# Performance work log

Measured on AMD Instinct MI355X. Metric: run time of the kernel, lower is better.

The kernel has to match this reference:

```python
import jax, jax.numpy as jnp
import numpy as np

BLANK = 59  # CFG['pad_phrase'] == blank_index == label pad value
NEG = jnp.float32(-1e30)  # -inf surrogate safe for logaddexp


def setup_inputs() -> dict:
    key = jax.random.key(0)
    k1, k2 = jax.random.split(key)
    B, T, V, L = 1024, 384, 60, 45
    labels = jax.random.randint(k1, (B, L), 0, BLANK, dtype=jnp.int32)
    logits = jax.random.normal(k2, (B, T, V), dtype=jnp.float32)
    return {"labels": labels, "logits": logits}


def _ctc_loss(logits, labels):
    # logits: [B, T, V] (not time-major), labels: [B, L] padded with BLANK
    B, T, V = logits.shape
    L = labels.shape[1]
    S = 2 * L + 1  # extended label length: blanks interleaved

    logp = jax.nn.log_softmax(logits, axis=-1)  # tf.nn.ctc_loss softmaxes internally

    # extended label sequence: [blank, l1, blank, l2, ..., blank]
    ext = jnp.full((B, S), BLANK, dtype=jnp.int32).at[:, 1::2].set(labels)
    # per-step emission log-probs for each extended-label position: [B, T, S]
    emit = jnp.take_along_axis(logp, ext[:, None, :], axis=2)

    # skip transition s-2 -> s allowed iff s >= 2, ext[s] != blank, ext[s] != ext[s-2]
    ext_m2 = jnp.pad(ext[:, :-2], ((0, 0), (2, 0)), constant_values=-1)
    skip_ok = (jnp.arange(S) >= 2) & (ext != BLANK) & (ext != ext_m2)

    # alpha init at t=0: only positions 0 (blank) and 1 (first label) reachable
    alpha0 = jnp.full((B, S), NEG).at[:, 0].set(emit[:, 0, 0]).at[:, 1].set(emit[:, 0, 1])

    def step(alpha, emit_t):
        s1 = jnp.pad(alpha[:, :-1], ((0, 0), (1, 0)), constant_values=NEG)
        s2 = jnp.where(skip_ok, jnp.pad(alpha[:, :-2], ((0, 0), (2, 0)), constant_values=NEG), NEG)
        alpha = jnp.logaddexp(jnp.logaddexp(alpha, s1), s2) + emit_t
        return alpha, None

    emit_tbs = jnp.swapaxes(emit, 0, 1)  # [T, B, S]
    alpha_T, _ = jax.lax.scan(step, alpha0, emit_tbs[1:])

    # label_length = number of non-pad tokens (as in the TF layer)
    label_len = jnp.sum((labels != BLANK).astype(jnp.int32), axis=-1)
    end = 2 * label_len  # index of final blank in extended sequence
    a_blank = jnp.take_along_axis(alpha_T, end[:, None], axis=1)[:, 0]
    a_label = jnp.take_along_axis(alpha_T, jnp.maximum(end - 1, 0)[:, None], axis=1)[:, 0]
    a_label = jnp.where(end > 0, a_label, NEG)
    nll = -jnp.logaddexp(a_blank, a_label)  # [B]
    return jnp.mean(nll)


def reference(labels, logits):
    return _ctc_loss(logits, labels)
```

## Files before the change

### kernel.cpp

```cpp
#include <hip/hip_runtime.h>
#include <hip/hip_fp16.h>

#define BLANKC 59

typedef _Float16 half8 __attribute__((ext_vector_type(8)));

__device__ __forceinline__ float wave_shr1(float x, float fill) {
    int r = __builtin_amdgcn_update_dpp(__float_as_int(fill), __float_as_int(x),
                                        0x138 , 0xF, 0xF, false);
    return __int_as_float(r);
}

template <int CTRL>
__device__ __forceinline__ float dpp_fmax(float x) {
    int r = __builtin_amdgcn_update_dpp(__float_as_int(x), __float_as_int(x),
                                        CTRL, 0xF, 0xF, false);
    return fmaxf(x, __int_as_float(r));
}

__device__ __forceinline__ float wave_max_bcast(float x) {
    x = dpp_fmax<0x111>(x);
    x = dpp_fmax<0x112>(x);
    x = dpp_fmax<0x114>(x);
    x = dpp_fmax<0x118>(x);
    x = dpp_fmax<0x142>(x);
    x = dpp_fmax<0x143>(x);
    return __int_as_float(__builtin_amdgcn_readlane(__float_as_int(x), 63));
}

#define TTILE 64
#define RS 392

__global__ __launch_bounds__(256)
void ctc_fused(const int* __restrict__ labels, const float* __restrict__ logits,
               float* __restrict__ out, int T, int V, int L, float inv_b) {
    const int b   = blockIdx.x;
    const int tid = threadIdx.x;

    __shared__ float  ftile[TTILE][61];
    __shared__ __half S[47 * RS];
    __shared__ int    labs[64];

    if (tid < 64) labs[tid] = (tid < L) ? labels[(long)b * L + tid] : BLANKC;
    for (int i = tid; i < T; i += 256) S[46 * RS + i] = __float2half(0.f);

    const float* src = logits + (long)b * T * V;
    const int ntile = T / TTILE;
    for (int tile = 0; tile < ntile; ++tile) {
        const float* s0 = src + (long)tile * TTILE * V;
        #pragma unroll
        for (int it = 0; it < 15; ++it) {
            const int idx = it * 256 + tid;
            const int r = idx / 60, c = idx - r * 60;
            ftile[r][c] = s0[idx];
        }
        __syncthreads();
        {
            const int t = tid >> 2;
            const int q = tid & 3;
            float s = 0.f;
            #pragma unroll
            for (int k = 0; k < 15; ++k) s += __expf(ftile[t][q * 15 + k]);
            s += __shfl_xor(s, 1, 64);
            s += __shfl_xor(s, 2, 64);
            const float lse = __logf(s);
            const int tg = tile * TTILE + t;
            #pragma unroll
            for (int j = 0; j < 12; ++j) {
                const int l = q * 12 + j;
                if (l < 46) {
                    const int v = (l < 45) ? labs[l] : BLANKC;
                    S[l * RS + tg] = __float2half(__expf(ftile[t][v] - lse));
                }
            }
        }
        __syncthreads();
    }

    if (tid >= 64) return;
    const int lane = tid;

    const int labL = (lane < L) ? labs[lane] : BLANKC;
    const int labP = (lane >= 1 && lane < L) ? labs[lane - 1] : BLANKC;
    const float skipf = ((lane >= 1) && (lane < L) && (labL != BLANKC) && (labL != labP))
                        ? 1.0f : 0.0f;

    unsigned long long mk = __ballot((lane < L) && (labL != BLANKC));
    const int len = __popcll(mk);

    const __half* zrow = &S[46 * RS];
    const __half* rowL = (lane < 45) ? &S[lane * RS] : zrow;
    const __half* rowB = (lane < 46) ? &S[45 * RS] : zrow;

    half8 curL = *(const half8*)(rowL);
    half8 curB = *(const half8*)(rowB);

    float a0 = (lane == 0) ? (float)curB[0] * 0x1p80f : 0.f;
    float a1 = (lane == 0) ? (float)curL[0] * 0x1p80f : 0.f;
    int esum = 80;

    auto step = [&](float eL, float eB) {
        const float p   = wave_shr1(a1, 0.0f);
        const float t1  = a0 + a1;
        const float na0 = (a0 + p) * eB;
        const float na1 = fmaf(skipf, p, t1) * eL;
        a0 = na0; a1 = na1;
    };

    auto renorm = [&]() {
        const float m = wave_max_bcast(fmaxf(a0, a1));
        const int e = (__float_as_int(m) >> 23) & 0xff;
        int sexp = 207 - e;
        if (sexp > 127) sexp = 127;
        const float sc = __int_as_float((sexp + 127) << 23);
        a0 *= sc; a1 *= sc;
        esum += sexp;
    };

    const int NSEG = T / 8;

    half8 nL = *(const half8*)(rowL + 8);
    half8 nB = *(const half8*)(rowB + 8);
    #pragma unroll
    for (int i = 1; i < 8; ++i) step((float)curL[i], (float)curB[i]);
    renorm();

    for (int c = 1; c < NSEG - 1; ++c) {
        const half8 cL = nL, cB = nB;
        nL = *(const half8*)(rowL + (c + 1) * 8);
        nB = *(const half8*)(rowB + (c + 1) * 8);
        #pragma unroll
        for (int i = 0; i < 8; ++i) step((float)cL[i], (float)cB[i]);
        renorm();
    }
    #pragma unroll
    for (int i = 0; i < 8; ++i) step((float)nL[i], (float)nB[i]);

    const float ab2 = __shfl(a0, len, 64);
    float al2 = __shfl(a1, (len > 0) ? len - 1 : 0, 64);
    al2 = (len > 0) ? al2 : 0.f;
    if (lane == 0) {
        const float s   = ab2 + al2;
        const float nll = -(__logf(s) - (float)esum * 0.69314718056f);
        atomicAdd(out, nll * inv_b);
    }
}

extern "C" void kernel_launch(void* const* d_in, const int* in_sizes, int n_in,
                              void* d_out, int out_size, void* d_ws, size_t ws_size,
                              hipStream_t stream) {
    const int* labels   = (const int*)d_in[0];
    const float* logits = (const float*)d_in[1];
    float* out          = (float*)d_out;
    (void)d_ws; (void)ws_size;

    const int L = 45, V = 60;
    const int B = in_sizes[0] / L;
    const int T = in_sizes[1] / (B * V);

    hipMemsetAsync(out, 0, (size_t)out_size * sizeof(float), stream);
    ctc_fused<<<B, 256, 0, stream>>>(labels, logits, out, T, V, L, 1.0f / (float)B);
}
```

Measured before the change: 170.9 us.

## Overlap alpha recursion scan with softmax/gather of next time tile

Restructures the kernel so wave 0 runs the CTC alpha recursion on the current 64-step tile while the whole block loads the next tile's logits into registers and computes log-softmax and the label gather into a double-buffered shared tile. Before, all emissions for the full sequence were computed first and the single-wave scan ran afterwards, leaving the other waves idle. The shared emission buffer also shrinks from the full T length to two 64-step tiles, which may raise occupancy. The cost is extra barriers per tile, and the scan in wave 0 now shares its critical path with the load and gather work in that same wave.

```diff
diff --git a/kernel.cpp b/kernel.cpp
--- a/kernel.cpp
+++ b/kernel.cpp
@@ -29,75 +29,66 @@
 }
 
 #define TTILE 64
-#define RS 392
+#define SDS 72
 
 __global__ __launch_bounds__(256)
 void ctc_fused(const int* __restrict__ labels, const float* __restrict__ logits,
                float* __restrict__ out, int T, int V, int L, float inv_b) {
-    const int b   = blockIdx.x;
-    const int tid = threadIdx.x;
+    const int b    = blockIdx.x;
+    const int tid  = threadIdx.x;
+    const int lane = tid & 63;
+    const int wid  = tid >> 6;
 
     __shared__ float  ftile[TTILE][61];
-    __shared__ __half S[47 * RS];
+    __shared__ __half Sd[2][47][SDS];
     __shared__ int    labs[64];
 
     if (tid < 64) labs[tid] = (tid < L) ? labels[(long)b * L + tid] : BLANKC;
-    for (int i = tid; i < T; i += 256) S[46 * RS + i] = __float2half(0.f);
+    if (tid < SDS) {
+        Sd[0][46][tid] = __float2half(0.f);
+        Sd[1][46][tid] = __float2half(0.f);
+    }
 
     const float* src = logits + (long)b * T * V;
     const int ntile = T / TTILE;
-    for (int tile = 0; tile < ntile; ++tile) {
-        const float* s0 = src + (long)tile * TTILE * V;
+
+    float rg[15];
+    auto load_tile = [&](int kt) {
+        const float* s0 = src + (long)kt * TTILE * V;
+        #pragma unroll
+        for (int it = 0; it < 15; ++it) rg[it] = s0[it * 256 + tid];
+    };
+    auto ftile_write = [&]() {
         #pragma unroll
         for (int it = 0; it < 15; ++it) {
             const int idx = it * 256 + tid;
             const int r = idx / 60, c = idx - r * 60;
-            ftile[r][c] = s0[idx];
+            ftile[r][c] = rg[it];
         }
-        __syncthreads();
-        {
-            const int t = tid >> 2;
-            const int q = tid & 3;
-            float s = 0.f;
-            #pragma unroll
-            for (int k = 0; k < 15; ++k) s += __expf(ftile[t][q * 15 + k]);
-            s += __shfl_xor(s, 1, 64);
-            s += __shfl_xor(s, 2, 64);
-            const float lse = __logf(s);
-            const int tg = tile * TTILE + t;
-            #pragma unroll
-            for (int j = 0; j < 12; ++j) {
-                const int l = q * 12 + j;
-                if (l < 46) {
-                    const int v = (l < 45) ? labs[l] : BLANKC;
-                    S[l * RS + tg] = __float2half(__expf(ftile[t][v] - lse));
-                }
+    };
+    auto lse_gather = [&](int nb) {
+        const int t = tid >> 2;
+        const int q = tid & 3;
+        float s = 0.f;
+        #pragma unroll
+        for (int k = 0; k < 15; ++k) s += __expf(ftile[t][q * 15 + k]);
+        s += __shfl_xor(s, 1, 64);
+        s += __shfl_xor(s, 2, 64);
+        const float lse = __logf(s);
+        #pragma unroll
+        for (int j = 0; j < 12; ++j) {
+            const int l = q * 12 + j;
+            if (l < 46) {
+                const int v = (l < 45) ? labs[l] : BLANKC;
+                Sd[nb][l][t] = __float2half(__expf(ftile[t][v] - lse));
             }
         }
-        __syncthreads();
-    }
+    };
 
-    if (tid >= 64) return;
-    const int lane = tid;
-
-    const int labL = (lane < L) ? labs[lane] : BLANKC;
-    const int labP = (lane >= 1 && lane < L) ? labs[lane - 1] : BLANKC;
-    const float skipf = ((lane >= 1) && (lane < L) && (labL != BLANKC) && (labL != labP))
-                        ? 1.0f : 0.0f;
-
-    unsigned long long mk = __ballot((lane < L) && (labL != BLANKC));
-    const int len = __popcll(mk);
-
-    const __half* zrow = &S[46 * RS];
-    const __half* rowL = (lane < 45) ? &S[lane * RS] : zrow;
-    const __half* rowB = (lane < 46) ? &S[45 * RS] : zrow;
-
-    half8 curL = *(const half8*)(rowL);
-    half8 curB = *(const half8*)(rowB);
-
-    float a0 = (lane == 0) ? (float)curB[0] * 0x1p80f : 0.f;
-    float a1 = (lane == 0) ? (float)curL[0] * 0x1p80f : 0.f;
-    int esum = 80;
+    float a0 = 0.f, a1 = 0.f;
+    int esum = 0;
+    float skipf = 0.f;
+    int len = 0, riL = 46, riB = 46;
 
     auto step = [&](float eL, float eB) {
         const float p   = wave_shr1(a1, 0.0f);
@@ -106,7 +97,6 @@
         const float na1 = fmaf(skipf, p, t1) * eL;
         a0 = na0; a1 = na1;
     };
-
     auto renorm = [&]() {
         const float m = wave_max_bcast(fmaxf(a0, a1));
         const int e = (__float_as_int(m) >> 23) & 0xff;
@@ -116,25 +106,67 @@
         a0 *= sc; a1 *= sc;
         esum += sexp;
     };
+    auto scan_tile = [&](int cb, bool first) {
+        const __half* rl = &Sd[cb][riL][0];
+        const __half* rb = &Sd[cb][riB][0];
+        half8 cL = *(const half8*)rl;
+        half8 cB = *(const half8*)rb;
+        half8 nL = *(const half8*)(rl + 8);
+        half8 nB = *(const half8*)(rb + 8);
+        if (first) {
+            a0 = (lane == 0) ? (float)cB[0] * 0x1p80f : 0.f;
+            a1 = (lane == 0) ? (float)cL[0] * 0x1p80f : 0.f;
+            esum = 80;
+            #pragma unroll
+            for (int i = 1; i < 8; ++i) step((float)cL[i], (float)cB[i]);
+        } else {
+            #pragma unroll
+            for (int i = 0; i < 8; ++i) step((float)cL[i], (float)cB[i]);
+        }
+        renorm();
+        #pragma unroll
+        for (int c = 1; c < 8; ++c) {
+            cL = nL; cB = nB;
+            if (c < 7) {
+                nL = *(const half8*)(rl + (c + 1) * 8);
+                nB = *(const half8*)(rb + (c + 1) * 8);
+            }
+            #pragma unroll
+            for (int i = 0; i < 8; ++i) step((float)cL[i], (float)cB[i]);
+            renorm();
+        }
+    };
 
-    const int NSEG = T / 8;
+    load_tile(0);
+    __syncthreads();
+    ftile_write();
+    __syncthreads();
+    lse_gather(0);
 
-    half8 nL = *(const half8*)(rowL + 8);
-    half8 nB = *(const half8*)(rowB + 8);
-    #pragma unroll
-    for (int i = 1; i < 8; ++i) step((float)curL[i], (float)curB[i]);
-    renorm();
+    {
+        const int labL = (lane < L) ? labs[lane] : BLANKC;
+        const int labP = (lane >= 1 && lane < L) ? labs[lane - 1] : BLANKC;
+        skipf = ((lane >= 1) && (lane < L) && (labL != BLANKC) && (labL != labP))
+                ? 1.0f : 0.0f;
+        const unsigned long long mk = __ballot((lane < L) && (labL != BLANKC));
+        len = __popcll(mk);
+        riL = (lane < 45) ? lane : 46;
+        riB = (lane < 46) ? 45 : 46;
+    }
+    __syncthreads();
 
-    for (int c = 1; c < NSEG - 1; ++c) {
-        const half8 cL = nL, cB = nB;
-        nL = *(const half8*)(rowL + (c + 1) * 8);
-        nB = *(const half8*)(rowB + (c + 1) * 8);
-        #pragma unroll
-        for (int i = 0; i < 8; ++i) step((float)cL[i], (float)cB[i]);
-        renorm();
+    int cur = 0;
+    for (int kt = 0; kt < ntile - 1; ++kt) {
+        load_tile(kt + 1);
+        if (wid == 0) scan_tile(cur, kt == 0);
+        ftile_write();
+        __syncthreads();
+        lse_gather(cur ^ 1);
+        __syncthreads();
+        cur ^= 1;
     }
-    #pragma unroll
-    for (int i = 0; i < 8; ++i) step((float)nL[i], (float)nB[i]);
+    if (wid != 0) return;
+    scan_tile(cur, ntile == 1);
 
     const float ab2 = __shfl(a0, len, 64);
     float al2 = __shfl(a1, (len > 0) ? len - 1 : 0, 64);
```

Result: faster. 153.3 us (-10.3%).

## Overlap softmax producer waves with CTC recursion via LDS flags

Applied to the files above, without the earlier changes.

Splits the block into three producer waves that compute softmax on 8-timestep chunks and one consumer wave that runs the alpha recursion as soon as each chunk is flagged ready, instead of finishing all softmax work before the serial recursion starts. The softmax uses a reciprocal and direct exp ratio instead of log/exp, vectorised float4 loads with register prefetch, and an XOR-swizzled emission layout to reduce bank conflicts. It adds spin-waiting on LDS atomics with memory fences, and hardcodes T=384 (NCH=48, 3 waves of 128 steps) and V=60.

```diff
diff --git a/kernel.cpp b/kernel.cpp
--- a/kernel.cpp
+++ b/kernel.cpp
@@ -4,6 +4,7 @@
 #define BLANKC 59
 
 typedef _Float16 half8 __attribute__((ext_vector_type(8)));
+typedef _Float16 half4 __attribute__((ext_vector_type(4)));
 
 __device__ __forceinline__ float wave_shr1(float x, float fill) {
     int r = __builtin_amdgcn_update_dpp(__float_as_int(fill), __float_as_int(x),
@@ -16,6 +17,13 @@
     int r = __builtin_amdgcn_update_dpp(__float_as_int(x), __float_as_int(x),
                                         CTRL, 0xF, 0xF, false);
     return fmaxf(x, __int_as_float(r));
+}
+
+template <int CTRL>
+__device__ __forceinline__ float dpp_addf(float x) {
+    int r = __builtin_amdgcn_update_dpp(__float_as_int(x), __float_as_int(x),
+                                        CTRL, 0xF, 0xF, false);
+    return x + __int_as_float(r);
 }
 
 __device__ __forceinline__ float wave_max_bcast(float x) {
@@ -28,76 +36,108 @@
     return __int_as_float(__builtin_amdgcn_readlane(__float_as_int(x), 63));
 }
 
-#define TTILE 64
-#define RS 392
+#define RS   392
+#define NCH  48
+#define SCRS 68
 
 __global__ __launch_bounds__(256)
 void ctc_fused(const int* __restrict__ labels, const float* __restrict__ logits,
                float* __restrict__ out, int T, int V, int L, float inv_b) {
-    const int b   = blockIdx.x;
-    const int tid = threadIdx.x;
-
-    __shared__ float  ftile[TTILE][61];
-    __shared__ __half S[47 * RS];
-    __shared__ int    labs[64];
+    const int b    = blockIdx.x;
+    const int tid  = threadIdx.x;
+    const int lane = tid & 63;
+    const int wid  = tid >> 6;
+
+    __shared__ __align__(16) __half S[46 * RS];
+    __shared__ __align__(16) __half scr[3][8][SCRS];
+    __shared__ int labs[64];
+    __shared__ int flags[4];
 
     if (tid < 64) labs[tid] = (tid < L) ? labels[(long)b * L + tid] : BLANKC;
-    for (int i = tid; i < T; i += 256) S[46 * RS + i] = __float2half(0.f);
-
-    const float* src = logits + (long)b * T * V;
-    const int ntile = T / TTILE;
-    for (int tile = 0; tile < ntile; ++tile) {
-        const float* s0 = src + (long)tile * TTILE * V;
+    if (tid < 4)  flags[tid] = 0;
+    __syncthreads();
+
+    if (wid != 0) {
+        const int w  = wid - 1;
+        const int tq = lane >> 3;
+        const int q  = lane & 7;
+        const int c0 = q * 8;
+        const bool full = (q < 7);
+        const float* src = logits + (long)b * T * V;
+
+        int gl[6], gr[6], gv[6]; bool gok[6];
         #pragma unroll
-        for (int it = 0; it < 15; ++it) {
-            const int idx = it * 256 + tid;
-            const int r = idx / 60, c = idx - r * 60;
-            ftile[r][c] = s0[idx];
-        }
-        __syncthreads();
-        {
-            const int t = tid >> 2;
-            const int q = tid & 3;
-            float s = 0.f;
+        for (int k = 0; k < 6; ++k) {
+            const int i = lane + (k << 6);
+            gok[k] = (i < 368);
+            gl[k] = i >> 3; gr[k] = i & 7;
+            const int ll = gok[k] ? gl[k] : 0;
+            gv[k] = (ll < 45) ? labs[ll] : BLANKC;
+        }
+
+        float4 A0, A1{0.f,0.f,0.f,0.f}, B0{0.f,0.f,0.f,0.f}, B1;
+        {   const float* p = src + (w * 128 + tq) * 60 + c0;
+            A0 = *(const float4*)p;
+            if (full) A1 = *(const float4*)(p + 4);
+        }
+        for (int pass = 0; pass < 16; ++pass) {
+            const int tbase = w * 128 + pass * 8;
+            B1 = float4{0.f,0.f,0.f,0.f};
+            if (pass < 15) {
+                const float* p = src + (tbase + 8 + tq) * 60 + c0;
+                B0 = *(const float4*)p;
+                if (full) B1 = *(const float4*)(p + 4);
+            }
+            const float e0 = __expf(A0.x), e1 = __expf(A0.y),
+                        e2 = __expf(A0.z), e3 = __expf(A0.w);
+            float e4 = 0.f, e5 = 0.f, e6 = 0.f, e7 = 0.f;
+            if (full) { e4 = __expf(A1.x); e5 = __expf(A1.y);
+                        e6 = __expf(A1.z); e7 = __expf(A1.w); }
+            float s = ((e0 + e1) + (e2 + e3)) + ((e4 + e5) + (e6 + e7));
+            s = dpp_addf<0xB1>(s);
+            s = dpp_addf<0x4E>(s);
+            s += __shfl_xor(s, 4, 64);
+            const float inv = __builtin_amdgcn_rcpf(s);
+            const half4 p0 = { (_Float16)(e0 * inv), (_Float16)(e1 * inv),
+                               (_Float16)(e2 * inv), (_Float16)(e3 * inv) };
+            const half4 p1 = { (_Float16)(e4 * inv), (_Float16)(e5 * inv),
+                               (_Float16)(e6 * inv), (_Float16)(e7 * inv) };
+            *(half4*)&scr[w][tq][c0]     = p0;
+            *(half4*)&scr[w][tq][c0 + 4] = p1;
+            __threadfence_block();
+
+            const int c = tbase >> 3;
             #pragma unroll
-            for (int k = 0; k < 15; ++k) s += __expf(ftile[t][q * 15 + k]);
-            s += __shfl_xor(s, 1, 64);
-            s += __shfl_xor(s, 2, 64);
-            const float lse = __logf(s);
-            const int tg = tile * TTILE + t;
-            #pragma unroll
-            for (int j = 0; j < 12; ++j) {
-                const int l = q * 12 + j;
-                if (l < 46) {
-                    const int v = (l < 45) ? labs[l] : BLANKC;
-                    S[l * RS + tg] = __float2half(__expf(ftile[t][v] - lse));
+            for (int k = 0; k < 6; ++k) {
+                if (gok[k]) {
+                    const int cp = c ^ ((gl[k] >> 3) & 7);
+                    S[gl[k] * RS + cp * 8 + gr[k]] = scr[w][gr[k]][gv[k]];
                 }
             }
-        }
-        __syncthreads();
+            __threadfence_block();
+            if (lane == 0)
+                __hip_atomic_fetch_add(&flags[w], 1, __ATOMIC_RELEASE,
+                                       __HIP_MEMORY_SCOPE_WORKGROUP);
+            A0 = B0; A1 = B1;
+        }
+        return;
     }
-
-    if (tid >= 64) return;
-    const int lane = tid;
 
     const int labL = (lane < L) ? labs[lane] : BLANKC;
     const int labP = (lane >= 1 && lane < L) ? labs[lane - 1] : BLANKC;
     const float skipf = ((lane >= 1) && (lane < L) && (labL != BLANKC) && (labL != labP))
                         ? 1.0f : 0.0f;
-
-    unsigned long long mk = __ballot((lane < L) && (labL != BLANKC));
+    const unsigned long long mk = __ballot((lane < L) && (labL != BLANKC));
     const int len = __popcll(mk);
 
-    const __half* zrow = &S[46 * RS];
-    const __half* rowL = (lane < 45) ? &S[lane * RS] : zrow;
-    const __half* rowB = (lane < 46) ? &S[45 * RS] : zrow;
-
-    half8 curL = *(const half8*)(rowL);
-    half8 curB = *(const half8*)(rowB);
-
-    float a0 = (lane == 0) ? (float)curB[0] * 0x1p80f : 0.f;
-    float a1 = (lane == 0) ? (float)curL[0] * 0x1p80f : 0.f;
-    int esum = 80;
+    const int rl = (lane < 45) ? lane : 45;
+    const __half* baseL = &S[rl * RS];
+    const __half* baseB = &S[45 * RS];
+    const int xL = (rl >> 3) & 7;
+    const int xB = 5;
+
+    float a0 = 0.f, a1 = 0.f;
+    int esum = 0;
 
     auto step = [&](float eL, float eB) {
         const float p   = wave_shr1(a1, 0.0f);
@@ -106,7 +146,6 @@
         const float na1 = fmaf(skipf, p, t1) * eL;
         a0 = na0; a1 = na1;
     };
-
     auto renorm = [&]() {
         const float m = wave_max_bcast(fmaxf(a0, a1));
         const int e = (__float_as_int(m) >> 23) & 0xff;
@@ -117,24 +156,46 @@
         esum += sexp;
     };
 
-    const int NSEG = T / 8;
-
-    half8 nL = *(const half8*)(rowL + 8);
-    half8 nB = *(const half8*)(rowB + 8);
-    #pragma unroll
-    for (int i = 1; i < 8; ++i) step((float)curL[i], (float)curB[i]);
-    renorm();
-
-    for (int c = 1; c < NSEG - 1; ++c) {
-        const half8 cL = nL, cB = nB;
-        nL = *(const half8*)(rowL + (c + 1) * 8);
-        nB = *(const half8*)(rowB + (c + 1) * 8);
-        #pragma unroll
-        for (int i = 0; i < 8; ++i) step((float)cL[i], (float)cB[i]);
+    int seen = 0, curw = -1;
+    auto waitc = [&](int c) {
+        const int w = c >> 4, pw = c & 15;
+        if (w != curw) {
+            curw = w;
+            seen = __hip_atomic_load(&flags[w], __ATOMIC_ACQUIRE,
+                                     __HIP_MEMORY_SCOPE_WORKGROUP);
+        }
+        while (seen <= pw) {
+            __builtin_amdgcn_s_sleep(2);
+            seen = __hip_atomic_load(&flags[curw], __ATOMIC_ACQUIRE,
+                                     __HIP_MEMORY_SCOPE_WORKGROUP);
+        }
+    };
+    const half8 hz = {};
+    auto loadch = [&](int c, half8& hL, half8& hB) {
+        hL = *(const half8*)(baseL + (c ^ xL) * 8);
+        hB = *(const half8*)(baseB + (c ^ xB) * 8);
+        if (lane >= 45) hL = hz;
+        if (lane >= 46) hB = hz;
+    };
+
+    half8 cL, cB, nL, nB;
+    waitc(0);
+    loadch(0, cL, cB);
+    for (int c = 0; c < NCH; ++c) {
+        if (c + 1 < NCH) { waitc(c + 1); loadch(c + 1, nL, nB); }
+        if (c == 0) {
+            a0 = (lane == 0) ? (float)cB[0] * 0x1p80f : 0.f;
+            a1 = (lane == 0) ? (float)cL[0] * 0x1p80f : 0.f;
+            esum = 80;
+            #pragma unroll
+            for (int i = 1; i < 8; ++i) step((float)cL[i], (float)cB[i]);
+        } else {
+            #pragma unroll
+            for (int i = 0; i < 8; ++i) step((float)cL[i], (float)cB[i]);
+        }
         renorm();
+        cL = nL; cB = nB;
     }
-    #pragma unroll
-    for (int i = 0; i < 8; ++i) step((float)nL[i], (float)nB[i]);
 
     const float ab2 = __shfl(a0, len, 64);
     float al2 = __shfl(a1, (len > 0) ? len - 1 : 0, 64);
```

After: 160.9 us. 1.06x faster.
